# Performance work log

Measured on AMD Instinct MI355X. Metric: run time of the kernel, lower is better.

The kernel has to match this reference:

```python
import jax, jax.numpy as jnp
import numpy as np


def setup_inputs() -> dict:
    B, n, emb, K = 8, 128, 256, 8
    N = B * n            # total nodes
    Eg = n               # edges per graph (one out-edge per node)
    E = B * Eg           # total edges
    E2 = E * K           # total edge-to-edge edges
    key = jax.random.key(0)
    k1, k2, k3, k4 = jax.random.split(key, 4)
    x = jax.random.normal(k1, (N, emb), jnp.float32)
    edge_attr = jax.random.normal(k2, (E, emb), jnp.float32)
    enc_W = jax.random.normal(k3, (3, emb), jnp.float32)
    e2e_W = jax.random.normal(k4, (3, emb), jnp.float32)
    # deterministic simple-graph edges: node i -> node (i+1) mod n within each graph
    e = np.arange(E); g = e // Eg; el = e % Eg
    src = g * n + el
    dst = g * n + (el + 1) % n
    edge_index = jnp.asarray(np.stack([src, dst]), jnp.int32)
    batch_vec = jnp.asarray(np.arange(N) // n, jnp.int32)
    # e2e graph: edge-node s connected to edge-nodes (s+1..s+K) mod Eg within graph
    f = np.arange(E2); fg = f // (Eg * K); fl = f % (Eg * K)
    s_e = fl % Eg; d_e = (s_e + 1 + fl // Eg) % Eg
    e2e_edge_index = jnp.asarray(np.stack([fg * Eg + s_e, fg * Eg + d_e]), jnp.int32)
    e_batch = jnp.asarray(np.arange(E) // Eg, jnp.int32)
    # each e2e edge carries features of the dst node of its source edge
    e2e_node_index = jnp.asarray(dst[fg * Eg + s_e], jnp.int32)
    return {"x": x, "edge_attr": edge_attr, "enc_W": enc_W, "e2e_W": e2e_W,
            "edge_index": edge_index, "batch_vec": batch_vec,
            "e2e_edge_index": e2e_edge_index, "e_batch": e_batch,
            "e2e_node_index": e2e_node_index, "n_graphs": B}


def _offsets(bvec, B):
    # start offset of each graph in the packed (node or edge) dimension
    counts = jax.ops.segment_sum(jnp.ones_like(bvec), bvec, num_segments=B)
    return jnp.concatenate([jnp.zeros((1,), counts.dtype), jnp.cumsum(counts)[:-1]])


def reference(x, edge_attr, enc_W, e2e_W, edge_index, batch_vec,
              e2e_edge_index, e_batch, e2e_node_index, n_graphs):
    B = int(n_graphs)
    N, emb = x.shape
    n = N // B
    E = edge_attr.shape[0]
    Eg = E // B
    mask = jnp.array([0.0, 1.0, 1.0], x.dtype)[:, None]  # Embedding padding_idx=0

    # ---- node-level dense edge features ----
    node_off = _offsets(batch_vec, B)
    src, dst = edge_index[0], edge_index[1]
    g = batch_vec[src]
    li = src - node_off[g]
    lj = dst - node_off[g]
    ea = edge_attr + x[src] + x[dst]                       # [E, emb]
    edge_dense = jnp.zeros((B, n, n, emb), x.dtype).at[g, li, lj].add(ea)
    # edge type codes: 0 = connected, 1 = diagonal, 2 = disconnected
    adj = jnp.zeros((B, n, n), jnp.int32).at[g, li, lj].add(2)
    lall = jnp.arange(N) - node_off[batch_vec]
    adj = adj.at[batch_vec, lall, lall].add(1)
    edge_dense = edge_dense + (enc_W * mask)[2 - adj]

    # ---- edge-to-edge dense features ----
    x2 = x + jax.ops.segment_sum(edge_attr, dst, num_segments=N)
    e_off = _offsets(e_batch, B)
    es, ed = e2e_edge_index[0], e2e_edge_index[1]
    eg = e_batch[es]
    eli = es - e_off[eg]
    elj = ed - e_off[eg]
    e2e_dense = jnp.zeros((B, Eg, Eg, emb), x.dtype).at[eg, eli, elj].add(x2[e2e_node_index])
    adj2 = jnp.zeros((B, Eg, Eg), jnp.int32).at[eg, eli, elj].add(2)
    leall = jnp.arange(E) - e_off[e_batch]
    adj2 = adj2.at[e_batch, leall, leall].add(1)
    e2e_dense = e2e_dense + (e2e_W * mask)[2 - adj2]

    return edge_dense, e2e_dense
```

## Files before the change

### kernel.cpp

```cpp
#include <hip/hip_runtime.h>

#define MAXB 1024
#define DIAGF 0x40000000

__global__ void offsets_k(const int* __restrict__ bv, int N,
                          const int* __restrict__ eb, int E,
                          const int* __restrict__ nG,
                          int* __restrict__ node_off, int* __restrict__ e_off) {
    __shared__ int c1[MAXB];
    __shared__ int c2[MAXB];
    int B = nG[0];
    if (B > MAXB) B = MAXB;
    for (int i = threadIdx.x; i < B; i += blockDim.x) { c1[i] = 0; c2[i] = 0; }
    __syncthreads();
    for (int i = threadIdx.x; i < N; i += blockDim.x) atomicAdd(&c1[bv[i]], 1);
    for (int i = threadIdx.x; i < E; i += blockDim.x) atomicAdd(&c2[eb[i]], 1);
    __syncthreads();
    if (threadIdx.x == 0) {
        int a = 0, b = 0;
        for (int g = 0; g < B; ++g) {
            node_off[g] = a; a += c1[g];
            e_off[g]    = b; b += c2[g];
        }
    }
}

__global__ void map_init_k(int* __restrict__ map, int C) {
    int stride = gridDim.x * blockDim.x;
    for (int i = blockIdx.x * blockDim.x + threadIdx.x; i < C; i += stride)
        map[i] = -1;
}

__global__ void map_diag_k(const int* __restrict__ nG, int N, int E,
                           int* __restrict__ map) {
    int t = blockIdx.x * blockDim.x + threadIdx.x;
    if (t >= N + E) return;
    int B = nG[0];
    int n = N / B, Eg = E / B;
    int C1 = N * n;
    int cell;
    if (t < N) {
        int g = t / n, l = t - g * n;
        cell = (g * n + l) * n + l;
    } else {
        int u = t - N;
        int g = u / Eg, l = u - g * Eg;
        cell = C1 + (g * Eg + l) * Eg + l;
    }
    map[cell] = -2;
}

__global__ void map_scatter_k(const int* __restrict__ ei,
                              const int* __restrict__ bv,
                              const int* __restrict__ node_off,
                              const int* __restrict__ e2e_ei,
                              const int* __restrict__ eb,
                              const int* __restrict__ e_off,
                              const int* __restrict__ nidx,
                              const int* __restrict__ nG,
                              int N, int E, int E2, int* __restrict__ map) {
    int t = blockIdx.x * blockDim.x + threadIdx.x;
    if (t >= E + E2) return;
    int B = nG[0];
    int n = N / B, Eg = E / B;
    int C1 = N * n;
    if (t < E) {
        int e = t;
        int s = ei[e], d = ei[E + e];
        int g = bv[s];
        int li = s - node_off[g], lj = d - node_off[g];
        map[(g * n + li) * n + lj] = e | (li == lj ? DIAGF : 0);
    } else {
        int f = t - E;
        int es = e2e_ei[f], ed = e2e_ei[E2 + f];
        int g = eb[es];
        int li = es - e_off[g], lj = ed - e_off[g];
        map[C1 + (g * Eg + li) * Eg + lj] = nidx[f] | (li == lj ? DIAGF : 0);
    }
}

__global__ void x2_copy_k(const float4* __restrict__ x, float4* __restrict__ x2, int n4) {
    int t = blockIdx.x * blockDim.x + threadIdx.x;
    if (t < n4) x2[t] = x[t];
}

__global__ void x2_add_k(const float* __restrict__ edge_attr,
                         const int* __restrict__ edge_index,
                         int E, int emb, float* __restrict__ x2) {
    int t = blockIdx.x * blockDim.x + threadIdx.x;
    if (t >= E * emb) return;
    int e = t / emb;
    int c = t - e * emb;
    int dst = edge_index[E + e];
    atomicAdd(&x2[dst * emb + c], edge_attr[t]);
}

__global__ __launch_bounds__(256) void main_k(
    const int* __restrict__ map,
    const float4* __restrict__ edge_attr,
    const float4* __restrict__ x,
    const float4* __restrict__ x2,
    const int* __restrict__ ei,
    const float4* __restrict__ encW,
    const float4* __restrict__ e2eW,
    const int* __restrict__ nG,
    int N, int E, int emb4, int C,
    float4* __restrict__ out) {
    int B = nG[0];
    int n = N / B;
    int C1 = N * n;
    int lane = threadIdx.x & 63;
    int wave = (blockIdx.x * blockDim.x + threadIdx.x) >> 6;
    int nw   = (gridDim.x * blockDim.x) >> 6;
    for (int cell = wave; cell < C; cell += nw) {
        int m = map[cell];
        const float4* W = (cell < C1) ? encW : e2eW;
        for (int c4 = lane; c4 < emb4; c4 += 64) {
            float4 v;
            if (m == -1) {
                v = W[2 * emb4 + c4];
            } else if (m == -2) {
                v = W[emb4 + c4];
            } else {
                int id = m & 0x3FFFFFFF;
                if (cell < C1) {
                    int s = ei[id], d = ei[E + id];
                    float4 a  = edge_attr[(long)id * emb4 + c4];
                    float4 xs = x[(long)s * emb4 + c4];
                    float4 xd = x[(long)d * emb4 + c4];
                    v.x = a.x + xs.x + xd.x;
                    v.y = a.y + xs.y + xd.y;
                    v.z = a.z + xs.z + xd.z;
                    v.w = a.w + xs.w + xd.w;
                } else {
                    v = x2[(long)id * emb4 + c4];
                }
                if (m & DIAGF) {
                    float4 w2 = W[2 * emb4 + c4];
                    v.x += w2.x; v.y += w2.y; v.z += w2.z; v.w += w2.w;
                }
            }
            out[(long)cell * emb4 + c4] = v;
        }
    }
}

extern "C" void kernel_launch(void* const* d_in, const int* in_sizes, int n_in,
                              void* d_out, int out_size, void* d_ws, size_t ws_size,
                              hipStream_t stream) {
    const float* x          = (const float*)d_in[0];
    const float* edge_attr  = (const float*)d_in[1];
    const float* enc_W      = (const float*)d_in[2];
    const float* e2e_W      = (const float*)d_in[3];
    const int* edge_index   = (const int*)d_in[4];
    const int* batch_vec    = (const int*)d_in[5];
    const int* e2e_ei       = (const int*)d_in[6];
    const int* e_batch      = (const int*)d_in[7];
    const int* e2e_nidx     = (const int*)d_in[8];
    const int* nG           = (const int*)d_in[9];

    int emb  = in_sizes[2] / 3;
    int emb4 = emb / 4;
    int N    = in_sizes[0] / emb;
    int E    = in_sizes[1] / emb;
    int E2   = in_sizes[8];
    int C    = out_size / emb;

    char* ws      = (char*)d_ws;
    int* node_off = (int*)ws;
    int* e_off    = (int*)(ws + 4096);
    float* x2     = (float*)(ws + 8192);
    int* map      = (int*)(ws + 8192 + (size_t)N * emb * 4);

    offsets_k<<<1, 256, 0, stream>>>(batch_vec, N, e_batch, E, nG, node_off, e_off);

    map_init_k<<<1024, 256, 0, stream>>>(map, C);

    map_diag_k<<<(N + E + 255) / 256, 256, 0, stream>>>(nG, N, E, map);

    map_scatter_k<<<(E + E2 + 255) / 256, 256, 0, stream>>>(
        edge_index, batch_vec, node_off, e2e_ei, e_batch, e_off,
        e2e_nidx, nG, N, E, E2, map);

    int n4x = (N * emb) / 4;
    x2_copy_k<<<(n4x + 255) / 256, 256, 0, stream>>>((const float4*)x, (float4*)x2, n4x);

    int tadd = E * emb;
    x2_add_k<<<(tadd + 255) / 256, 256, 0, stream>>>(edge_attr, edge_index, E, emb, x2);

    main_k<<<8192, 256, 0, stream>>>(
        map, (const float4*)edge_attr, (const float4*)x, (const float4*)x2,
        edge_index, (const float4*)enc_W, (const float4*)e2e_W,
        nG, N, E, emb4, C, (float4*)d_out);
}
```

Measured before the change: 292.8 us.

## Fuse prep kernels into two launches and use nontemporal output stores

Merges the six preprocessing kernels into two grid-stride kernels. prep1 does the offsets, the map initialisation and the x2 copy; prep2 does the diagonal marking, the edge scatter and the x2 atomic accumulation. Diagonal marking now uses atomicCAS(-1 to -2), so it cannot overwrite a scattered edge entry when both run in the same kernel without ordering. The large output write in main_k becomes a nontemporal store to cut cache pollution, and fusing cuts launch and inter-kernel gap overhead.

```diff
diff --git a/kernel.cpp b/kernel.cpp
--- a/kernel.cpp
+++ b/kernel.cpp
@@ -3,96 +3,93 @@
 #define MAXB 1024
 #define DIAGF 0x40000000
 
-__global__ void offsets_k(const int* __restrict__ bv, int N,
-                          const int* __restrict__ eb, int E,
-                          const int* __restrict__ nG,
-                          int* __restrict__ node_off, int* __restrict__ e_off) {
-    __shared__ int c1[MAXB];
-    __shared__ int c2[MAXB];
-    int B = nG[0];
-    if (B > MAXB) B = MAXB;
-    for (int i = threadIdx.x; i < B; i += blockDim.x) { c1[i] = 0; c2[i] = 0; }
-    __syncthreads();
-    for (int i = threadIdx.x; i < N; i += blockDim.x) atomicAdd(&c1[bv[i]], 1);
-    for (int i = threadIdx.x; i < E; i += blockDim.x) atomicAdd(&c2[eb[i]], 1);
-    __syncthreads();
-    if (threadIdx.x == 0) {
-        int a = 0, b = 0;
-        for (int g = 0; g < B; ++g) {
-            node_off[g] = a; a += c1[g];
-            e_off[g]    = b; b += c2[g];
+typedef float nat_f4 __attribute__((ext_vector_type(4)));
+
+__global__ void prep1_k(const int* __restrict__ bv, int N,
+                        const int* __restrict__ eb, int E,
+                        const int* __restrict__ nG,
+                        int* __restrict__ node_off, int* __restrict__ e_off,
+                        int* __restrict__ map, int C,
+                        const float4* __restrict__ x, float4* __restrict__ x2,
+                        int n4) {
+    if (blockIdx.x == 0) {
+        __shared__ int c1[MAXB];
+        __shared__ int c2[MAXB];
+        int B = nG[0];
+        if (B > MAXB) B = MAXB;
+        for (int i = threadIdx.x; i < B; i += blockDim.x) { c1[i] = 0; c2[i] = 0; }
+        __syncthreads();
+        for (int i = threadIdx.x; i < N; i += blockDim.x) atomicAdd(&c1[bv[i]], 1);
+        for (int i = threadIdx.x; i < E; i += blockDim.x) atomicAdd(&c2[eb[i]], 1);
+        __syncthreads();
+        if (threadIdx.x == 0) {
+            int a = 0, b = 0;
+            for (int g = 0; g < B; ++g) {
+                node_off[g] = a; a += c1[g];
+                e_off[g]    = b; b += c2[g];
+            }
         }
     }
+    int stride = gridDim.x * blockDim.x;
+    int t0 = blockIdx.x * blockDim.x + threadIdx.x;
+    for (int i = t0; i < C; i += stride) map[i] = -1;
+    for (int i = t0; i < n4; i += stride) x2[i] = x[i];
 }
 
-__global__ void map_init_k(int* __restrict__ map, int C) {
-    int stride = gridDim.x * blockDim.x;
-    for (int i = blockIdx.x * blockDim.x + threadIdx.x; i < C; i += stride)
-        map[i] = -1;
-}
-
-__global__ void map_diag_k(const int* __restrict__ nG, int N, int E,
-                           int* __restrict__ map) {
-    int t = blockIdx.x * blockDim.x + threadIdx.x;
-    if (t >= N + E) return;
+__global__ void prep2_k(const int* __restrict__ ei,
+                        const int* __restrict__ bv,
+                        const int* __restrict__ node_off,
+                        const int* __restrict__ e2e_ei,
+                        const int* __restrict__ eb,
+                        const int* __restrict__ e_off,
+                        const int* __restrict__ nidx,
+                        const int* __restrict__ nG,
+                        const float* __restrict__ edge_attr,
+                        float* __restrict__ x2,
+                        int N, int E, int E2, int emb,
+                        int* __restrict__ map) {
     int B = nG[0];
     int n = N / B, Eg = E / B;
     int C1 = N * n;
-    int cell;
-    if (t < N) {
-        int g = t / n, l = t - g * n;
-        cell = (g * n + l) * n + l;
-    } else {
-        int u = t - N;
-        int g = u / Eg, l = u - g * Eg;
-        cell = C1 + (g * Eg + l) * Eg + l;
+    int stride = gridDim.x * blockDim.x;
+    int t0 = blockIdx.x * blockDim.x + threadIdx.x;
+
+    for (int t = t0; t < N + E; t += stride) {
+        int cell;
+        if (t < N) {
+            int g = t / n, l = t - g * n;
+            cell = (g * n + l) * n + l;
+        } else {
+            int u = t - N;
+            int g = u / Eg, l = u - g * Eg;
+            cell = C1 + (g * Eg + l) * Eg + l;
+        }
+        atomicCAS(&map[cell], -1, -2);
     }
-    map[cell] = -2;
-}
 
-__global__ void map_scatter_k(const int* __restrict__ ei,
-                              const int* __restrict__ bv,
-                              const int* __restrict__ node_off,
-                              const int* __restrict__ e2e_ei,
-                              const int* __restrict__ eb,
-                              const int* __restrict__ e_off,
-                              const int* __restrict__ nidx,
-                              const int* __restrict__ nG,
-                              int N, int E, int E2, int* __restrict__ map) {
-    int t = blockIdx.x * blockDim.x + threadIdx.x;
-    if (t >= E + E2) return;
-    int B = nG[0];
-    int n = N / B, Eg = E / B;
-    int C1 = N * n;
-    if (t < E) {
-        int e = t;
-        int s = ei[e], d = ei[E + e];
-        int g = bv[s];
-        int li = s - node_off[g], lj = d - node_off[g];
-        map[(g * n + li) * n + lj] = e | (li == lj ? DIAGF : 0);
-    } else {
-        int f = t - E;
-        int es = e2e_ei[f], ed = e2e_ei[E2 + f];
-        int g = eb[es];
-        int li = es - e_off[g], lj = ed - e_off[g];
-        map[C1 + (g * Eg + li) * Eg + lj] = nidx[f] | (li == lj ? DIAGF : 0);
+    for (int t = t0; t < E + E2; t += stride) {
+        if (t < E) {
+            int e = t;
+            int s = ei[e], d = ei[E + e];
+            int g = bv[s];
+            int li = s - node_off[g], lj = d - node_off[g];
+            map[(g * n + li) * n + lj] = e | (li == lj ? DIAGF : 0);
+        } else {
+            int f = t - E;
+            int es = e2e_ei[f], ed = e2e_ei[E2 + f];
+            int g = eb[es];
+            int li = es - e_off[g], lj = ed - e_off[g];
+            map[C1 + (g * Eg + li) * Eg + lj] = nidx[f] | (li == lj ? DIAGF : 0);
+        }
     }
-}
 
-__global__ void x2_copy_k(const float4* __restrict__ x, float4* __restrict__ x2, int n4) {
-    int t = blockIdx.x * blockDim.x + threadIdx.x;
-    if (t < n4) x2[t] = x[t];
-}
-
-__global__ void x2_add_k(const float* __restrict__ edge_attr,
-                         const int* __restrict__ edge_index,
-                         int E, int emb, float* __restrict__ x2) {
-    int t = blockIdx.x * blockDim.x + threadIdx.x;
-    if (t >= E * emb) return;
-    int e = t / emb;
-    int c = t - e * emb;
-    int dst = edge_index[E + e];
-    atomicAdd(&x2[dst * emb + c], edge_attr[t]);
+    int T3 = E * emb;
+    for (int t = t0; t < T3; t += stride) {
+        int e = t / emb;
+        int c = t - e * emb;
+        int dst = ei[E + e];
+        atomicAdd(&x2[dst * emb + c], edge_attr[t]);
+    }
 }
 
 __global__ __launch_bounds__(256) void main_k(
@@ -140,7 +137,9 @@
                     v.x += w2.x; v.y += w2.y; v.z += w2.z; v.w += w2.w;
                 }
             }
-            out[(long)cell * emb4 + c4] = v;
+            nat_f4 nv;
+            nv.x = v.x; nv.y = v.y; nv.z = v.z; nv.w = v.w;
+            __builtin_nontemporal_store(nv, (nat_f4*)&out[(long)cell * emb4 + c4]);
         }
     }
 }
@@ -172,21 +171,14 @@
     float* x2     = (float*)(ws + 8192);
     int* map      = (int*)(ws + 8192 + (size_t)N * emb * 4);
 
-    offsets_k<<<1, 256, 0, stream>>>(batch_vec, N, e_batch, E, nG, node_off, e_off);
+    int n4x = (N * emb) / 4;
+    prep1_k<<<1024, 256, 0, stream>>>(batch_vec, N, e_batch, E, nG,
+                                      node_off, e_off, map, C,
+                                      (const float4*)x, (float4*)x2, n4x);
 
-    map_init_k<<<1024, 256, 0, stream>>>(map, C);
-
-    map_diag_k<<<(N + E + 255) / 256, 256, 0, stream>>>(nG, N, E, map);
-
-    map_scatter_k<<<(E + E2 + 255) / 256, 256, 0, stream>>>(
-        edge_index, batch_vec, node_off, e2e_ei, e_batch, e_off,
-        e2e_nidx, nG, N, E, E2, map);
-
-    int n4x = (N * emb) / 4;
-    x2_copy_k<<<(n4x + 255) / 256, 256, 0, stream>>>((const float4*)x, (float4*)x2, n4x);
-
-    int tadd = E * emb;
-    x2_add_k<<<(tadd + 255) / 256, 256, 0, stream>>>(edge_attr, edge_index, E, emb, x2);
+    prep2_k<<<1024, 256, 0, stream>>>(edge_index, batch_vec, node_off,
+                                      e2e_ei, e_batch, e_off, e2e_nidx, nG,
+                                      edge_attr, x2, N, E, E2, emb, map);
 
     main_k<<<8192, 256, 0, stream>>>(
         map, (const float4*)edge_attr, (const float4*)x, (const float4*)x2,
```

Measured after the change: 292.4 us. About the same (-0.1%).
